# Kernel tuning notes

Measured on AMD Instinct MI355X. Metric: run time of the kernel, lower is better.

Reference implementation:

```python
import jax, jax.numpy as jnp
import numpy as np

NEG_SLOPE = 0.01

def lrelu(x):
    return jax.nn.leaky_relu(x, NEG_SLOPE)

def lin(x, w, b):
    # torch Linear: x @ W.T + b, W shape (out, in)
    return x @ w.T + b

def meansum_pool(mask, x_local, *x_global):
    # masked sum + mean over points, concat with global/context vectors
    x_sum = (x_local * mask).sum(axis=1)                 # (b, d)
    x_mean = x_sum / mask.sum(axis=1)                    # (b, d) / (b, 1)
    return jnp.concatenate([x_mean, x_sum, *x_global], axis=1)


def setup_inputs() -> dict:
    key = jax.random.key(0)
    ks = jax.random.split(key, 16)
    B, N, DIN, DC, H, G, NB, DOUT = 16, 8192, 3, 16, 128, 10, 6, 3

    def w(k, shape, fan_in):
        return (jax.random.normal(k, shape, jnp.float32) / np.float32(np.sqrt(fan_in)))

    inp = {
        "x_local": jax.random.normal(ks[0], (B, N, DIN), jnp.float32),
        "context": jax.random.normal(ks[1], (B, DC), jnp.float32),
        "mask": (jax.random.uniform(ks[2], (B, N, 1)) < 0.9).astype(jnp.float32),
        # EPiC_Projection params (effective weight-normed weights)
        "proj_lw": w(ks[3], (H, DIN), DIN), "proj_lb": jnp.zeros((H,), jnp.float32),
        "proj_g0w": w(ks[4], (H, 2 * H + DC), 2 * H + DC), "proj_g0b": jnp.zeros((H,), jnp.float32),
        "proj_g1w": w(ks[5], (H, H), H), "proj_g1b": jnp.zeros((H,), jnp.float32),
        "proj_g2w": w(ks[6], (G, H), H), "proj_g2b": jnp.zeros((G,), jnp.float32),
        # stacked per-block EPiC_layer params
        "g1w": w(ks[7], (NB, H, 2 * H + G + DC), 2 * H + G + DC), "g1b": jnp.zeros((NB, H), jnp.float32),
        "g2w": w(ks[8], (NB, G, H), H), "g2b": jnp.zeros((NB, G), jnp.float32),
        "l1w": w(ks[9], (NB, H, H + G + DC), H + G + DC), "l1b": jnp.zeros((NB, H), jnp.float32),
        "l2w": w(ks[10], (NB, H, H), H), "l2b": jnp.zeros((NB, H), jnp.float32),
        # output head
        "outw": w(ks[11], (DOUT, H), H), "outb": jnp.zeros((DOUT,), jnp.float32),
    }
    return inp


def reference(x_local, context, mask,
              proj_lw, proj_lb, proj_g0w, proj_g0b, proj_g1w, proj_g1b, proj_g2w, proj_g2b,
              g1w, g1b, g2w, g2b, l1w, l1b, l2w, l2b, outw, outb):
    B, N, _ = x_local.shape
    # --- EPiC_Projection ---
    xl = lrelu(lin(x_local, proj_lw, proj_lb))           # (b, n, H)
    xg = meansum_pool(mask, xl, context)                 # (b, 2H + DC)
    xg = lrelu(lin(xg, proj_g0w, proj_g0b))
    xg = lrelu(lin(xg, proj_g1w, proj_g1b))
    xg = lrelu(lin(xg, proj_g2w, proj_g2b))              # (b, G)
    xl = xl * mask
    # --- EPiC layers (no skip: use_skip_connection=False -> +0) ---
    num_blocks = g1w.shape[0]
    for i in range(num_blocks):
        pooled = meansum_pool(mask, xl, xg, context)     # (b, 2H + G + DC)
        h_g = lrelu(lin(pooled, g1w[i], g1b[i]))
        xg = lrelu(lin(h_g, g2w[i], g2b[i]) + xg)        # residual global
        xg_b = jnp.broadcast_to(xg[:, None, :], (B, N, xg.shape[-1]))
        ctx_b = jnp.broadcast_to(context[:, None, :], (B, N, context.shape[-1]))
        cat = jnp.concatenate([xl, xg_b, ctx_b], axis=2)  # (b, n, H + G + DC)
        h_l = lrelu(lin(cat, l1w[i], l1b[i]))
        xl = lrelu(lin(h_l, l2w[i], l2b[i]) + xl) * mask  # residual local, masked
    h = lin(xl, outw, outb)                              # (b, n, 3)
    return h * mask
```

## Files before the change

### kernel.cpp

```cpp
#include <hip/hip_runtime.h>
#include <hip/hip_bf16.h>


typedef __attribute__((ext_vector_type(8))) short short8;
typedef __attribute__((ext_vector_type(4))) float f32x4;

#define B_ 16
#define N_ 8192
#define DC_ 16
#define H_ 128
#define G_ 10
#define NB_ 6
#define NEG_ 0.01f

__device__ __forceinline__ float lrelu(float x) { return x > 0.f ? x : NEG_ * x; }

__device__ __forceinline__ unsigned short f2bf(float x) {
  union { float f; unsigned u; } v; v.f = x;
  return (unsigned short)((v.u + 0x7fffu + ((v.u >> 16) & 1u)) >> 16);
}
__device__ __forceinline__ float bf2f(unsigned short u) {
  union { unsigned u; float f; } v; v.u = ((unsigned)u) << 16; return v.f;
}
__device__ __forceinline__ void split_bf(float x, unsigned short& h, unsigned short& l) {
  union { float f; unsigned u; } v; v.f = x;
  unsigned hu = v.u & 0xffff0000u;
  h = (unsigned short)(hu >> 16);
  union { unsigned u; float f; } hv; hv.u = hu;
  l = f2bf(x - hv.f);
}

__device__ __forceinline__ f32x4 mfma16(short8 a, short8 b, f32x4 c) {
  return __builtin_amdgcn_mfma_f32_16x16x32_bf16(a, b, c, 0, 0, 0);
}

__device__ __forceinline__ void make_frags(f32x4 v0, f32x4 v1, short8& bh, short8& bl) {
  unsigned short h, l;
#pragma unroll
  for (int j = 0; j < 4; ++j) {
    split_bf(v0[j], h, l);
    bh[j] = (short)h; bl[j] = (short)l;
  }
#pragma unroll
  for (int j = 0; j < 4; ++j) {
    split_bf(v1[j], h, l);
    bh[4 + j] = (short)h; bl[4 + j] = (short)l;
  }
}

__device__ __forceinline__ void async_cp16(const void* g, void* l) {
  __builtin_amdgcn_global_load_lds(
      (const __attribute__((address_space(1))) void*)g,
      (__attribute__((address_space(3))) void*)l, 16, 0, 0);
}

__device__ __forceinline__ void agent_store(float* p, float v) {
  __hip_atomic_store(p, v, __ATOMIC_RELAXED, __HIP_MEMORY_SCOPE_AGENT);
}
__device__ __forceinline__ float agent_load(const float* p) {
  return __hip_atomic_load(p, __ATOMIC_RELAXED, __HIP_MEMORY_SCOPE_AGENT);
}

template <int NS>
__device__ void epic_global_tail(
    int b, int tid, const float* __restrict__ pP, float cnt,
    const float* __restrict__ xg_cur, float* __restrict__ xg_next,
    const float* __restrict__ context,
    const float* __restrict__ g1w_n, const float* __restrict__ g1b_n,
    const float* __restrict__ g2w_n, const float* __restrict__ g2b_n,
    const float* __restrict__ l1w_n, const float* __restrict__ l1b_n,
    float* __restrict__ gbias_out, float* shx) {
  if (tid < 256) {
    const int f = tid & 127, kh = tid >> 7;
    const float* pr = pP + ((size_t)b * NS + kh * (NS / 2)) * 128 + f;
    float s = 0.f;
#pragma unroll 8
    for (int w = 0; w < NS / 2; ++w) s += agent_load(pr + w * 128);
    shx[tid] = s;
  }
  __syncthreads();
  if (tid < 128) {
    float s = shx[tid] + shx[tid + 128];
    shx[384 + tid] = s;
    shx[256 + tid] = s / cnt;
  }
  if (tid < G_) shx[512 + tid] = xg_cur[tid];
  if (tid >= 32 && tid < 32 + DC_) shx[522 + tid - 32] = context[b * DC_ + tid - 32];
  __syncthreads();
  if (tid < 256) {
    const int f = tid & 127, kh = tid >> 7;
    const float* wr = g1w_n + (size_t)f * 282 + kh * 142;
    const float* vp = shx + 256 + kh * 142;
    const int n2 = kh ? 70 : 71;
    float a = 0.f;
#pragma unroll 8
    for (int j = 0; j < n2; ++j) {
      float2 w2 = *(const float2*)(wr + 2 * j);
      a += w2.x * vp[2 * j] + w2.y * vp[2 * j + 1];
    }
    shx[tid] = a;
  }
  __syncthreads();
  if (tid < 128) shx[544 + tid] = lrelu(shx[tid] + shx[tid + 128] + g1b_n[tid]);
  __syncthreads();
  if (tid < G_) {
    const float* wr = g2w_n + tid * 128;
    float a = g2b_n[tid] + shx[512 + tid];
#pragma unroll 8
    for (int j = 0; j < 32; ++j) {
      float4 w4 = *(const float4*)(wr + 4 * j);
      a += w4.x * shx[544 + 4 * j] + w4.y * shx[544 + 4 * j + 1] +
           w4.z * shx[544 + 4 * j + 2] + w4.w * shx[544 + 4 * j + 3];
    }
    float v = lrelu(a);
    shx[672 + tid] = v;
    xg_next[tid] = v;
  }
  __syncthreads();
  if (tid < 128) {
    const float* wr = l1w_n + tid * 154;
    float a = l1b_n[tid];
#pragma unroll
    for (int j = 0; j < G_; ++j) a += wr[128 + j] * shx[672 + j];
#pragma unroll
    for (int j = 0; j < DC_; ++j) a += wr[138 + j] * shx[522 + j];
    gbias_out[tid] = a;
  }
}

__global__ __launch_bounds__(256) void prep_weights(
    const float* __restrict__ l1w, const float* __restrict__ l2w,
    unsigned short* __restrict__ w1h, unsigned short* __restrict__ w1l,
    unsigned short* __restrict__ w2h, unsigned short* __restrict__ w2l,
    unsigned int* __restrict__ counters) {
  int idx = blockIdx.x * 256 + threadIdx.x;
  const int total = NB_ * H_ * H_;
  if (idx < 112) counters[idx] = 0u;
  if (idx < total) {
    int i = idx / (H_ * H_), rem = idx % (H_ * H_);
    int F = rem / H_, k = rem % H_;
    int mt = F >> 4, r = F & 15, ks = k >> 5, c = k & 31;
    int off = i * 16384 + (mt * 4 + ks) * 512 + ((c >> 3) * 16 + r) * 8 + (c & 7);
    unsigned short h, l;
    split_bf(l1w[(i * H_ + F) * 154 + k], h, l);
    w1h[off] = h; w1l[off] = l;
    split_bf(l2w[(i * H_ + F) * H_ + k], h, l);
    w2h[off] = h; w2l[off] = l;
  }
}

__global__ __launch_bounds__(256, 2) void proj_local_kernel(
    const float* __restrict__ xloc, const float* __restrict__ maskp,
    const float* __restrict__ plw, const float* __restrict__ plb,
    float* __restrict__ xlf, float* __restrict__ pP,
    float* __restrict__ cntp, float* __restrict__ cnt_g,
    unsigned int* __restrict__ counters,
    const float* __restrict__ context,
    const float* __restrict__ g0w, const float* __restrict__ g0b,
    const float* __restrict__ g1pw, const float* __restrict__ g1pb,
    const float* __restrict__ g2pw, const float* __restrict__ g2pb,
    float* __restrict__ xg_g,
    const float* __restrict__ g1w0, const float* __restrict__ g1b0,
    const float* __restrict__ g2w0, const float* __restrict__ g2b0,
    const float* __restrict__ l1w0, const float* __restrict__ l1b0,
    float* __restrict__ gbias_g) {
  __shared__ float wq[H_][4];
  __shared__ float wsum[512];
  __shared__ float cw[4];
  __shared__ float shx[768];
  __shared__ int winflag;
  const int tid = threadIdx.x, bid = blockIdx.x;
  const int wv = tid >> 6, lane = tid & 63;
  const int q = lane >> 4, n16 = lane & 15;
  const int b = bid >> 6;
  if (tid < H_) {
    wq[tid][0] = plw[tid * 3 + 0];
    wq[tid][1] = plw[tid * 3 + 1];
    wq[tid][2] = plw[tid * 3 + 2];
    wq[tid][3] = plb[tid];
  }
  __syncthreads();
  const int t = bid * 4 + wv;
  const int p0 = t * 32;
  const int pa = p0 + n16, pb = p0 + 16 + n16;
  const float xa0 = xloc[pa * 3], xa1 = xloc[pa * 3 + 1], xa2 = xloc[pa * 3 + 2];
  const float xb0 = xloc[pb * 3], xb1 = xloc[pb * 3 + 1], xb2 = xloc[pb * 3 + 2];
  const float m0 = maskp[pa], m1 = maskp[pb];
  float* ga = xlf + (size_t)(2 * t) * 2048;
  float* gb = ga + 2048;
#pragma unroll
  for (int ms = 0; ms < 8; ++ms) {
    f32x4 v0, v1;
#pragma unroll
    for (int r = 0; r < 4; ++r) {
      const int F = ms * 16 + q * 4 + r;
      float4 w4 = *(const float4*)wq[F];
      v0[r] = lrelu(w4.x * xa0 + w4.y * xa1 + w4.z * xa2 + w4.w) * m0;
      v1[r] = lrelu(w4.x * xb0 + w4.y * xb1 + w4.z * xb2 + w4.w) * m1;
    }
    *(f32x4*)(ga + ms * 256 + (q * 16 + n16) * 4) = v0;
    *(f32x4*)(gb + ms * 256 + (q * 16 + n16) * 4) = v1;
    f32x4 s = v0 + v1;
#pragma unroll
    for (int r = 0; r < 4; ++r) {
      float sv = s[r];
      sv += __shfl_xor(sv, 1, 64);
      sv += __shfl_xor(sv, 2, 64);
      sv += __shfl_xor(sv, 4, 64);
      sv += __shfl_xor(sv, 8, 64);
      s[r] = sv;
    }
    if (n16 == 0) *(f32x4*)&wsum[wv * 128 + ms * 16 + q * 4] = s;
  }
  {
    float c = (q == 0) ? (m0 + m1) : 0.f;
    c += __shfl_xor(c, 1, 64);
    c += __shfl_xor(c, 2, 64);
    c += __shfl_xor(c, 4, 64);
    c += __shfl_xor(c, 8, 64);
    if (lane == 0) cw[wv] = c;
  }
  __syncthreads();
  if (tid < 128) {
    agent_store(&pP[(size_t)(2 * bid) * 128 + tid], wsum[tid] + wsum[128 + tid]);
    agent_store(&pP[(size_t)(2 * bid + 1) * 128 + tid], wsum[256 + tid] + wsum[384 + tid]);
  }
  if (tid == 0) agent_store(&cntp[bid], cw[0] + cw[1] + cw[2] + cw[3]);

  __syncthreads();
  if (tid == 0) winflag = (atomicAdd(&counters[b], 1u) == 63u) ? 1 : 0;
  __syncthreads();
  if (!winflag) return;
  if (tid < 64) shx[688 + tid] = agent_load(&cntp[b * 64 + tid]);
  __syncthreads();
  if (tid == 0) {
    float c = 0.f;
#pragma unroll
    for (int w = 0; w < 64; ++w) c += shx[688 + w];
    shx[752] = c;
    cnt_g[b] = c;
  }
  __syncthreads();
  const float cnt = shx[752];
  {
    const int f = tid & 127, kh = tid >> 7;
    const float* pr = pP + ((size_t)b * 128 + kh * 64) * 128 + f;
    float s = 0.f;
#pragma unroll 8
    for (int w = 0; w < 64; ++w) s += agent_load(pr + w * 128);
    shx[tid] = s;
  }
  __syncthreads();
  if (tid < 128) {
    float s = shx[tid] + shx[tid + 128];
    shx[384 + tid] = s;
    shx[256 + tid] = s / cnt;
  }
  if (tid < DC_) shx[512 + tid] = context[b * DC_ + tid];
  __syncthreads();
  {
    const int f = tid & 127, kh = tid >> 7;
    const float* wr = g0w + (size_t)f * 272 + kh * 136;
    const float* vp = shx + 256 + kh * 136;
    float a = 0.f;
#pragma unroll 8
    for (int j = 0; j < 34; ++j) {
      float4 w4 = *(const float4*)(wr + 4 * j);
      a += w4.x * vp[4 * j] + w4.y * vp[4 * j + 1] + w4.z * vp[4 * j + 2] + w4.w * vp[4 * j + 3];
    }
    __syncthreads();
    shx[tid] = a;
  }
  __syncthreads();
  if (tid < 128) shx[544 + tid] = lrelu(shx[tid] + shx[tid + 128] + g0b[tid]);
  __syncthreads();
  {
    const int f = tid & 127, kh = tid >> 7;
    const float* wr = g1pw + (size_t)f * 128 + kh * 64;
    const float* vp = shx + 544 + kh * 64;
    float a = 0.f;
#pragma unroll 8
    for (int j = 0; j < 16; ++j) {
      float4 w4 = *(const float4*)(wr + 4 * j);
      a += w4.x * vp[4 * j] + w4.y * vp[4 * j + 1] + w4.z * vp[4 * j + 2] + w4.w * vp[4 * j + 3];
    }
    __syncthreads();
    shx[tid] = a;
  }
  __syncthreads();
  if (tid < 128) shx[544 + tid] = lrelu(shx[tid] + shx[tid + 128] + g1pb[tid]);
  __syncthreads();
  if (tid < G_) {
    const float* wr = g2pw + tid * 128;
    float a = g2pb[tid];
#pragma unroll 8
    for (int j = 0; j < 32; ++j) {
      float4 w4 = *(const float4*)(wr + 4 * j);
      a += w4.x * shx[544 + 4 * j] + w4.y * shx[544 + 4 * j + 1] +
           w4.z * shx[544 + 4 * j + 2] + w4.w * shx[544 + 4 * j + 3];
    }
    xg_g[(0 * 16 + b) * 16 + tid] = lrelu(a);
  }
  __syncthreads();
  epic_global_tail<128>(b, tid, pP, cnt,
                        xg_g + (0 * 16 + b) * 16, xg_g + (1 * 16 + b) * 16, context,
                        g1w0, g1b0, g2w0, g2b0, l1w0, l1b0,
                        gbias_g + (size_t)(0 * 16 + b) * 128, shx);
}

template <bool LAST>
__global__ __launch_bounds__(512, 2) void epic_local_kernel(
    float* __restrict__ xlf, float* __restrict__ pP,
    const float* __restrict__ cnt_g, unsigned int* __restrict__ counters_blk,
    const float* __restrict__ gbias_in,
    const float* __restrict__ xg_tail_cur, float* __restrict__ xg_tail_next,
    float* __restrict__ gbias_tail_out,
    const float* __restrict__ context,
    const float* __restrict__ g1w_n, const float* __restrict__ g1b_n,
    const float* __restrict__ g2w_n, const float* __restrict__ g2b_n,
    const float* __restrict__ l1w_n, const float* __restrict__ l1b_n,
    const float* __restrict__ l2b,
    const unsigned short* __restrict__ w1h, const unsigned short* __restrict__ w1l,
    const unsigned short* __restrict__ w2h, const unsigned short* __restrict__ w2l,
    const float* __restrict__ maskp,
    const float* __restrict__ outw, const float* __restrict__ outb,
    float* __restrict__ outp) {
  __shared__ unsigned short wbuf[65536];
  __shared__ float tiles[8][576];
  __shared__ float shx[768];
  __shared__ float gbias_s[128];
  __shared__ float l2b_s[128];
  __shared__ float wsum[1024];
  __shared__ float outw_s[392];
  __shared__ int winflag;
  const int tid = threadIdx.x, bid = blockIdx.x;
  const int b = bid >> 5;
  const int wv = tid >> 6, lane = tid & 63;
  const int q = lane >> 4, n16 = lane & 15;

  {
    const unsigned short* src =
        (wv < 2) ? w1h : (wv < 4) ? w1l : (wv < 6) ? w2h : w2l;
    const char* s8 = (const char*)(src + (wv & 1) * 8192) + lane * 16;
    char* d8 = (char*)wbuf + wv * 16384;
#pragma unroll
    for (int j = 0; j < 16; ++j) async_cp16(s8 + j * 1024, d8 + j * 1024);
  }
  if (tid < 128) {
    gbias_s[tid] = gbias_in[b * 128 + tid];
    l2b_s[tid] = l2b[tid];
  }
  if (LAST) {
    if (tid < 384) outw_s[tid] = outw[tid];
    if (tid >= 384 && tid < 387) outw_s[tid] = outb[tid - 384];
  }

  const int g0i = bid * 16 + wv * 2;
  short8 xbh[2][4], xbl[2][4];
#pragma unroll
  for (int nt = 0; nt < 2; ++nt) {
    const float* base_nt = xlf + (size_t)(g0i + nt) * 2048;
#pragma unroll
    for (int ks = 0; ks < 4; ++ks) {
      const float* pb = base_nt + (2 * ks + (q >> 1)) * 256 + ((q & 1) * 32 + n16) * 4;
      f32x4 v0 = *(const f32x4*)pb;
      f32x4 v1 = *(const f32x4*)(pb + 64);
      make_frags(v0, v1, xbh[nt][ks], xbl[nt][ks]);
    }
  }
  __syncthreads();

  const unsigned short* w1h_l = wbuf;
  const unsigned short* w1l_l = wbuf + 16384;
  const unsigned short* w2h_l = wbuf + 32768;
  const unsigned short* w2l_l = wbuf + 49152;
  float* T = tiles[wv];
  const int lane16 = lane * 8;

  f32x4 acc2[2][8];
#pragma unroll
  for (int nt = 0; nt < 2; ++nt)
#pragma unroll
    for (int ms = 0; ms < 8; ++ms) acc2[nt][ms] = (f32x4){0.f, 0.f, 0.f, 0.f};

#pragma unroll
  for (int ko = 0; ko < 4; ++ko) {
    f32x4 acc[2][2];
#pragma unroll
    for (int nt = 0; nt < 2; ++nt)
#pragma unroll
      for (int msl = 0; msl < 2; ++msl) acc[nt][msl] = (f32x4){0.f, 0.f, 0.f, 0.f};
#pragma unroll
    for (int msl = 0; msl < 2; ++msl) {
      short8 a1h[4], a1l[4];
#pragma unroll
      for (int ks = 0; ks < 4; ++ks) {
        const int off = ((ko * 2 + msl) * 4 + ks) * 512 + lane16;
        a1h[ks] = *(const short8*)(w1h_l + off);
        a1l[ks] = *(const short8*)(w1l_l + off);
      }
#pragma unroll
      for (int ks = 0; ks < 4; ++ks)
#pragma unroll
        for (int nt = 0; nt < 2; ++nt) {
          acc[nt][msl] = mfma16(a1h[ks], xbh[nt][ks], acc[nt][msl]);
          acc[nt][msl] = mfma16(a1l[ks], xbh[nt][ks], acc[nt][msl]);
          acc[nt][msl] = mfma16(a1h[ks], xbl[nt][ks], acc[nt][msl]);
        }
    }
    short8 b2h[2], b2l[2];
#pragma unroll
    for (int nt = 0; nt < 2; ++nt) {
#pragma unroll
      for (int msl = 0; msl < 2; ++msl) {
        f32x4 gb4 = *(const f32x4*)&gbias_s[(ko * 2 + msl) * 16 + q * 4];
        f32x4 hv;
#pragma unroll
        for (int r = 0; r < 4; ++r) hv[r] = lrelu(acc[nt][msl][r] + gb4[r]);
        *(f32x4*)&T[n16 * 36 + msl * 16 + q * 4] = hv;
      }
      __builtin_amdgcn_wave_barrier();
      {
        f32x4 h0 = *(const f32x4*)&T[n16 * 36 + q * 8];
        f32x4 h1 = *(const f32x4*)&T[n16 * 36 + q * 8 + 4];
        make_frags(h0, h1, b2h[nt], b2l[nt]);
      }
      __builtin_amdgcn_wave_barrier();
    }
#pragma unroll
    for (int half = 0; half < 2; ++half) {
      short8 a2h[4], a2l[4];
#pragma unroll
      for (int mi = 0; mi < 4; ++mi) {
        const int off = ((half * 4 + mi) * 4 + ko) * 512 + lane16;
        a2h[mi] = *(const short8*)(w2h_l + off);
        a2l[mi] = *(const short8*)(w2l_l + off);
      }
#pragma unroll
      for (int mi = 0; mi < 4; ++mi)
#pragma unroll
        for (int nt = 0; nt < 2; ++nt) {
          acc2[nt][half * 4 + mi] = mfma16(a2h[mi], b2h[nt], acc2[nt][half * 4 + mi]);
          acc2[nt][half * 4 + mi] = mfma16(a2l[mi], b2h[nt], acc2[nt][half * 4 + mi]);
          acc2[nt][half * 4 + mi] = mfma16(a2h[mi], b2l[nt], acc2[nt][half * 4 + mi]);
        }
    }
  }

  float mk[2];
#pragma unroll
  for (int nt = 0; nt < 2; ++nt) mk[nt] = maskp[(g0i + nt) * 16 + n16];
  f32x4 vsum[8];
  float po[2][3];
  if (!LAST) {
#pragma unroll
    for (int ms = 0; ms < 8; ++ms) vsum[ms] = (f32x4){0.f, 0.f, 0.f, 0.f};
  } else {
#pragma unroll
    for (int nt = 0; nt < 2; ++nt) po[nt][0] = po[nt][1] = po[nt][2] = 0.f;
  }
#pragma unroll
  for (int nt = 0; nt < 2; ++nt) {
    float* base_nt = xlf + (size_t)(g0i + nt) * 2048;
#pragma unroll
    for (int ms = 0; ms < 8; ++ms) {
      f32x4 lb4 = *(const f32x4*)&l2b_s[ms * 16 + q * 4];
      float* xo = base_nt + ms * 256 + (q * 16 + n16) * 4;
      f32x4 old = *(const f32x4*)xo;
      f32x4 v;
#pragma unroll
      for (int r = 0; r < 4; ++r) v[r] = lrelu(acc2[nt][ms][r] + lb4[r] + old[r]) * mk[nt];
      if (!LAST) {
        *(f32x4*)xo = v;
        vsum[ms] += v;
      } else {
        f32x4 w0 = *(const f32x4*)&outw_s[0 * 128 + ms * 16 + q * 4];
        f32x4 w1 = *(const f32x4*)&outw_s[1 * 128 + ms * 16 + q * 4];
        f32x4 w2 = *(const f32x4*)&outw_s[2 * 128 + ms * 16 + q * 4];
#pragma unroll
        for (int r = 0; r < 4; ++r) {
          po[nt][0] += v[r] * w0[r];
          po[nt][1] += v[r] * w1[r];
          po[nt][2] += v[r] * w2[r];
        }
      }
    }
  }
  if (LAST) {
#pragma unroll
    for (int nt = 0; nt < 2; ++nt)
#pragma unroll
      for (int o = 0; o < 3; ++o) {
        float s = po[nt][o];
        s += __shfl_xor(s, 16, 64);
        s += __shfl_xor(s, 32, 64);
        po[nt][o] = s;
      }
    if (q == 0) {
#pragma unroll
      for (int nt = 0; nt < 2; ++nt) {
        const int p = (g0i + nt) * 16 + n16;
#pragma unroll
        for (int o = 0; o < 3; ++o)
          outp[(size_t)p * 3 + o] = (po[nt][o] + outw_s[384 + o]) * mk[nt];
      }
    }
    return;
  }
#pragma unroll
  for (int ms = 0; ms < 8; ++ms) {
    f32x4 sr;
#pragma unroll
    for (int r = 0; r < 4; ++r) {
      float s = vsum[ms][r];
      s += __shfl_xor(s, 1, 64);
      s += __shfl_xor(s, 2, 64);
      s += __shfl_xor(s, 4, 64);
      s += __shfl_xor(s, 8, 64);
      sr[r] = s;
    }
    if (n16 == 0) *(f32x4*)&wsum[wv * 128 + ms * 16 + q * 4] = sr;
  }
  __syncthreads();
  if (tid < 128) {
    float s = 0.f;
#pragma unroll
    for (int w = 0; w < 8; ++w) s += wsum[w * 128 + tid];
    agent_store(&pP[(size_t)bid * 128 + tid], s);
  }

  __syncthreads();
  if (tid == 0) winflag = (atomicAdd(&counters_blk[b], 1u) == 31u) ? 1 : 0;
  __syncthreads();
  if (!winflag) return;
  epic_global_tail<32>(b, tid, pP, cnt_g[b], xg_tail_cur + b * 16, xg_tail_next + b * 16,
                       context, g1w_n, g1b_n, g2w_n, g2b_n, l1w_n, l1b_n,
                       gbias_tail_out + (size_t)b * 128, shx);
}

extern "C" void kernel_launch(void* const* d_in, const int* in_sizes, int n_in,
                              void* d_out, int out_size, void* d_ws, size_t ws_size,
                              hipStream_t stream) {
  const float* x_local = (const float*)d_in[0];
  const float* context = (const float*)d_in[1];
  const float* mask = (const float*)d_in[2];
  const float* proj_lw = (const float*)d_in[3];
  const float* proj_lb = (const float*)d_in[4];
  const float* proj_g0w = (const float*)d_in[5];
  const float* proj_g0b = (const float*)d_in[6];
  const float* proj_g1w = (const float*)d_in[7];
  const float* proj_g1b = (const float*)d_in[8];
  const float* proj_g2w = (const float*)d_in[9];
  const float* proj_g2b = (const float*)d_in[10];
  const float* g1w = (const float*)d_in[11];
  const float* g1b = (const float*)d_in[12];
  const float* g2w = (const float*)d_in[13];
  const float* g2b = (const float*)d_in[14];
  const float* l1w = (const float*)d_in[15];
  const float* l1b = (const float*)d_in[16];
  const float* l2w = (const float*)d_in[17];
  const float* l2b = (const float*)d_in[18];
  const float* outw = (const float*)d_in[19];
  const float* outb = (const float*)d_in[20];
  float* out = (float*)d_out;

  char* ws = (char*)d_ws;
  float* xlf = (float*)ws;
  float* pP = (float*)(ws + 67108864);
  float* cntp = (float*)(ws + 68157440);
  float* cnt_g = (float*)(ws + 68161536);
  float* xg_g = (float*)(ws + 68161600);
  float* gbias_g = (float*)(ws + 68168768);
  unsigned int* counters = (unsigned int*)(ws + 68217920);
  unsigned short* w1h = (unsigned short*)(ws + 68218368);
  unsigned short* w1l = (unsigned short*)(ws + 68414976);
  unsigned short* w2h = (unsigned short*)(ws + 68611584);
  unsigned short* w2l = (unsigned short*)(ws + 68808192);

  prep_weights<<<384, 256, 0, stream>>>(l1w, l2w, w1h, w1l, w2h, w2l, counters);
  proj_local_kernel<<<1024, 256, 0, stream>>>(
      x_local, mask, proj_lw, proj_lb, xlf, pP, cntp, cnt_g, counters, context,
      proj_g0w, proj_g0b, proj_g1w, proj_g1b, proj_g2w, proj_g2b, xg_g,
      g1w, g1b, g2w, g2b, l1w, l1b, gbias_g);
  for (int i = 0; i < NB_; ++i) {
    const int j = i + 1;
    const float* g1w_n = g1w + (size_t)j * 128 * 282;
    const float* g1b_n = g1b + j * 128;
    const float* g2w_n = g2w + j * 10 * 128;
    const float* g2b_n = g2b + j * 10;
    const float* l1w_n = l1w + (size_t)j * 128 * 154;
    const float* l1b_n = l1b + j * 128;
    const unsigned short* w1h_i = w1h + i * 16384;
    const unsigned short* w1l_i = w1l + i * 16384;
    const unsigned short* w2h_i = w2h + i * 16384;
    const unsigned short* w2l_i = w2l + i * 16384;
    if (i == NB_ - 1) {
      epic_local_kernel<true><<<512, 512, 0, stream>>>(
          xlf, pP, cnt_g, counters + (i + 1) * 16, gbias_g + (size_t)(i * 16) * 128,
          nullptr, nullptr, nullptr, context,
          nullptr, nullptr, nullptr, nullptr, nullptr, nullptr,
          l2b + i * 128, w1h_i, w1l_i, w2h_i, w2l_i, mask, outw, outb, out);
    } else {
      epic_local_kernel<false><<<512, 512, 0, stream>>>(
          xlf, pP, cnt_g, counters + (i + 1) * 16, gbias_g + (size_t)(i * 16) * 128,
          xg_g + (i + 1) * 16 * 16, xg_g + (i + 2) * 16 * 16,
          gbias_g + (size_t)((i + 1) * 16) * 128, context,
          g1w_n, g1b_n, g2w_n, g2b_n, l1w_n, l1b_n,
          l2b + i * 128, w1h_i, w1l_i, w2h_i, w2l_i, mask, outw, outb, out);
    }
  }
}
```

Baseline: 477.1 us.

## Process two point tiles per block and pass hidden layer via cross-lane shuffles

Halves the grid so each block loops over two 256-point tiles, amortizing the 128KB LDS weight load and reducing global partial sums and atomic counters per batch. The first GEMM now computes all 8 output tiles before the second GEMM, and the intermediate activations are redistributed between MFMA layouts with __shfl instead of a per-wave LDS tile, removing the tiles buffer and its wave barriers. This raises register pressure (full acc[2][8] plus b2 fragments) and adds many shuffle instructions, and the smaller grid means fewer blocks to hide latency.

```diff
diff --git a/kernel.cpp b/kernel.cpp
--- a/kernel.cpp
+++ b/kernel.cpp
@@ -326,7 +326,6 @@
     const float* __restrict__ outw, const float* __restrict__ outb,
     float* __restrict__ outp) {
   __shared__ unsigned short wbuf[65536];
-  __shared__ float tiles[8][576];
   __shared__ float shx[768];
   __shared__ float gbias_s[128];
   __shared__ float l2b_s[128];
@@ -334,7 +333,7 @@
   __shared__ float outw_s[392];
   __shared__ int winflag;
   const int tid = threadIdx.x, bid = blockIdx.x;
-  const int b = bid >> 5;
+  const int b = bid >> 4;
   const int wv = tid >> 6, lane = tid & 63;
   const int q = lane >> 4, n16 = lane & 15;
 
@@ -354,159 +353,173 @@
     if (tid < 384) outw_s[tid] = outw[tid];
     if (tid >= 384 && tid < 387) outw_s[tid] = outb[tid - 384];
   }
-
-  const int g0i = bid * 16 + wv * 2;
-  short8 xbh[2][4], xbl[2][4];
-#pragma unroll
-  for (int nt = 0; nt < 2; ++nt) {
-    const float* base_nt = xlf + (size_t)(g0i + nt) * 2048;
-#pragma unroll
-    for (int ks = 0; ks < 4; ++ks) {
-      const float* pb = base_nt + (2 * ks + (q >> 1)) * 256 + ((q & 1) * 32 + n16) * 4;
-      f32x4 v0 = *(const f32x4*)pb;
-      f32x4 v1 = *(const f32x4*)(pb + 64);
-      make_frags(v0, v1, xbh[nt][ks], xbl[nt][ks]);
-    }
-  }
   __syncthreads();
 
   const unsigned short* w1h_l = wbuf;
   const unsigned short* w1l_l = wbuf + 16384;
   const unsigned short* w2h_l = wbuf + 32768;
   const unsigned short* w2l_l = wbuf + 49152;
-  float* T = tiles[wv];
   const int lane16 = lane * 8;
-
-  f32x4 acc2[2][8];
-#pragma unroll
-  for (int nt = 0; nt < 2; ++nt)
-#pragma unroll
-    for (int ms = 0; ms < 8; ++ms) acc2[nt][ms] = (f32x4){0.f, 0.f, 0.f, 0.f};
-
-#pragma unroll
-  for (int ko = 0; ko < 4; ++ko) {
-    f32x4 acc[2][2];
+  const int srcA = 2 * (q & 1) * 16 + n16;
+  const bool sel = (q >> 1) != 0;
+
+  f32x4 vsum[8];
+  if (!LAST) {
+#pragma unroll
+    for (int ms = 0; ms < 8; ++ms) vsum[ms] = (f32x4){0.f, 0.f, 0.f, 0.f};
+  }
+
+#pragma unroll
+  for (int it = 0; it < 2; ++it) {
+    const int g0i = (bid * 2 + it) * 16 + wv * 2;
+
+    short8 xbh[2][4], xbl[2][4];
+#pragma unroll
+    for (int nt = 0; nt < 2; ++nt) {
+      const float* base_nt = xlf + (size_t)(g0i + nt) * 2048;
+#pragma unroll
+      for (int ks = 0; ks < 4; ++ks) {
+        const float* pb = base_nt + (2 * ks + (q >> 1)) * 256 + ((q & 1) * 32 + n16) * 4;
+        f32x4 v0 = *(const f32x4*)pb;
+        f32x4 v1 = *(const f32x4*)(pb + 64);
+        make_frags(v0, v1, xbh[nt][ks], xbl[nt][ks]);
+      }
+    }
+
+    f32x4 acc[2][8];
 #pragma unroll
     for (int nt = 0; nt < 2; ++nt)
 #pragma unroll
-      for (int msl = 0; msl < 2; ++msl) acc[nt][msl] = (f32x4){0.f, 0.f, 0.f, 0.f};
-#pragma unroll
-    for (int msl = 0; msl < 2; ++msl) {
-      short8 a1h[4], a1l[4];
+      for (int mt = 0; mt < 8; ++mt) acc[nt][mt] = (f32x4){0.f, 0.f, 0.f, 0.f};
+#pragma unroll
+    for (int mt = 0; mt < 8; ++mt) {
+      short8 ah[4], al[4];
 #pragma unroll
       for (int ks = 0; ks < 4; ++ks) {
-        const int off = ((ko * 2 + msl) * 4 + ks) * 512 + lane16;
-        a1h[ks] = *(const short8*)(w1h_l + off);
-        a1l[ks] = *(const short8*)(w1l_l + off);
+        const int off = (mt * 4 + ks) * 512 + lane16;
+        ah[ks] = *(const short8*)(w1h_l + off);
+        al[ks] = *(const short8*)(w1l_l + off);
       }
 #pragma unroll
       for (int ks = 0; ks < 4; ++ks)
 #pragma unroll
         for (int nt = 0; nt < 2; ++nt) {
-          acc[nt][msl] = mfma16(a1h[ks], xbh[nt][ks], acc[nt][msl]);
-          acc[nt][msl] = mfma16(a1l[ks], xbh[nt][ks], acc[nt][msl]);
-          acc[nt][msl] = mfma16(a1h[ks], xbl[nt][ks], acc[nt][msl]);
+          acc[nt][mt] = mfma16(ah[ks], xbh[nt][ks], acc[nt][mt]);
+          acc[nt][mt] = mfma16(al[ks], xbh[nt][ks], acc[nt][mt]);
+          acc[nt][mt] = mfma16(ah[ks], xbl[nt][ks], acc[nt][mt]);
         }
     }
-    short8 b2h[2], b2l[2];
+
+#pragma unroll
+    for (int mt = 0; mt < 8; ++mt) {
+      f32x4 gb4 = *(const f32x4*)&gbias_s[mt * 16 + q * 4];
+#pragma unroll
+      for (int nt = 0; nt < 2; ++nt)
+#pragma unroll
+        for (int r = 0; r < 4; ++r) acc[nt][mt][r] = lrelu(acc[nt][mt][r] + gb4[r]);
+    }
+
+    short8 b2h[2][4], b2l[2][4];
+#pragma unroll
+    for (int nt = 0; nt < 2; ++nt)
+#pragma unroll
+      for (int ks = 0; ks < 4; ++ks) {
+        f32x4 f0, f1;
+#pragma unroll
+        for (int r = 0; r < 4; ++r) {
+          float a0 = __shfl(acc[nt][2 * ks][r], srcA, 64);
+          float a1 = __shfl(acc[nt][2 * ks + 1][r], srcA, 64);
+          f0[r] = sel ? a1 : a0;
+          float c0 = __shfl(acc[nt][2 * ks][r], srcA + 16, 64);
+          float c1 = __shfl(acc[nt][2 * ks + 1][r], srcA + 16, 64);
+          f1[r] = sel ? c1 : c0;
+        }
+        make_frags(f0, f1, b2h[nt][ks], b2l[nt][ks]);
+      }
+
+    f32x4 acc2[2][8];
+#pragma unroll
+    for (int nt = 0; nt < 2; ++nt)
+#pragma unroll
+      for (int mt = 0; mt < 8; ++mt) acc2[nt][mt] = (f32x4){0.f, 0.f, 0.f, 0.f};
+#pragma unroll
+    for (int mt = 0; mt < 8; ++mt) {
+      short8 ah[4], al[4];
+#pragma unroll
+      for (int ks = 0; ks < 4; ++ks) {
+        const int off = (mt * 4 + ks) * 512 + lane16;
+        ah[ks] = *(const short8*)(w2h_l + off);
+        al[ks] = *(const short8*)(w2l_l + off);
+      }
+#pragma unroll
+      for (int ks = 0; ks < 4; ++ks)
+#pragma unroll
+        for (int nt = 0; nt < 2; ++nt) {
+          acc2[nt][mt] = mfma16(ah[ks], b2h[nt][ks], acc2[nt][mt]);
+          acc2[nt][mt] = mfma16(al[ks], b2h[nt][ks], acc2[nt][mt]);
+          acc2[nt][mt] = mfma16(ah[ks], b2l[nt][ks], acc2[nt][mt]);
+        }
+    }
+
+    float mk[2];
+#pragma unroll
+    for (int nt = 0; nt < 2; ++nt) mk[nt] = maskp[(g0i + nt) * 16 + n16];
+    float po[2][3];
+    if (LAST) {
+#pragma unroll
+      for (int nt = 0; nt < 2; ++nt) po[nt][0] = po[nt][1] = po[nt][2] = 0.f;
+    }
 #pragma unroll
     for (int nt = 0; nt < 2; ++nt) {
-#pragma unroll
-      for (int msl = 0; msl < 2; ++msl) {
-        f32x4 gb4 = *(const f32x4*)&gbias_s[(ko * 2 + msl) * 16 + q * 4];
-        f32x4 hv;
-#pragma unroll
-        for (int r = 0; r < 4; ++r) hv[r] = lrelu(acc[nt][msl][r] + gb4[r]);
-        *(f32x4*)&T[n16 * 36 + msl * 16 + q * 4] = hv;
-      }
-      __builtin_amdgcn_wave_barrier();
-      {
-        f32x4 h0 = *(const f32x4*)&T[n16 * 36 + q * 8];
-        f32x4 h1 = *(const f32x4*)&T[n16 * 36 + q * 8 + 4];
-        make_frags(h0, h1, b2h[nt], b2l[nt]);
-      }
-      __builtin_amdgcn_wave_barrier();
-    }
-#pragma unroll
-    for (int half = 0; half < 2; ++half) {
-      short8 a2h[4], a2l[4];
-#pragma unroll
-      for (int mi = 0; mi < 4; ++mi) {
-        const int off = ((half * 4 + mi) * 4 + ko) * 512 + lane16;
-        a2h[mi] = *(const short8*)(w2h_l + off);
-        a2l[mi] = *(const short8*)(w2l_l + off);
-      }
-#pragma unroll
-      for (int mi = 0; mi < 4; ++mi)
-#pragma unroll
-        for (int nt = 0; nt < 2; ++nt) {
-          acc2[nt][half * 4 + mi] = mfma16(a2h[mi], b2h[nt], acc2[nt][half * 4 + mi]);
-          acc2[nt][half * 4 + mi] = mfma16(a2l[mi], b2h[nt], acc2[nt][half * 4 + mi]);
-          acc2[nt][half * 4 + mi] = mfma16(a2h[mi], b2l[nt], acc2[nt][half * 4 + mi]);
-        }
-    }
-  }
-
-  float mk[2];
-#pragma unroll
-  for (int nt = 0; nt < 2; ++nt) mk[nt] = maskp[(g0i + nt) * 16 + n16];
-  f32x4 vsum[8];
-  float po[2][3];
-  if (!LAST) {
-#pragma unroll
-    for (int ms = 0; ms < 8; ++ms) vsum[ms] = (f32x4){0.f, 0.f, 0.f, 0.f};
-  } else {
-#pragma unroll
-    for (int nt = 0; nt < 2; ++nt) po[nt][0] = po[nt][1] = po[nt][2] = 0.f;
-  }
-#pragma unroll
-  for (int nt = 0; nt < 2; ++nt) {
-    float* base_nt = xlf + (size_t)(g0i + nt) * 2048;
-#pragma unroll
-    for (int ms = 0; ms < 8; ++ms) {
-      f32x4 lb4 = *(const f32x4*)&l2b_s[ms * 16 + q * 4];
-      float* xo = base_nt + ms * 256 + (q * 16 + n16) * 4;
-      f32x4 old = *(const f32x4*)xo;
-      f32x4 v;
-#pragma unroll
-      for (int r = 0; r < 4; ++r) v[r] = lrelu(acc2[nt][ms][r] + lb4[r] + old[r]) * mk[nt];
-      if (!LAST) {
-        *(f32x4*)xo = v;
-        vsum[ms] += v;
-      } else {
-        f32x4 w0 = *(const f32x4*)&outw_s[0 * 128 + ms * 16 + q * 4];
-        f32x4 w1 = *(const f32x4*)&outw_s[1 * 128 + ms * 16 + q * 4];
-        f32x4 w2 = *(const f32x4*)&outw_s[2 * 128 + ms * 16 + q * 4];
-#pragma unroll
-        for (int r = 0; r < 4; ++r) {
-          po[nt][0] += v[r] * w0[r];
-          po[nt][1] += v[r] * w1[r];
-          po[nt][2] += v[r] * w2[r];
+      float* base_nt = xlf + (size_t)(g0i + nt) * 2048;
+#pragma unroll
+      for (int ms = 0; ms < 8; ++ms) {
+        f32x4 lb4 = *(const f32x4*)&l2b_s[ms * 16 + q * 4];
+        float* xo = base_nt + ms * 256 + (q * 16 + n16) * 4;
+        f32x4 old = *(const f32x4*)xo;
+        f32x4 v;
+#pragma unroll
+        for (int r = 0; r < 4; ++r) v[r] = lrelu(acc2[nt][ms][r] + lb4[r] + old[r]) * mk[nt];
+        if (!LAST) {
+          *(f32x4*)xo = v;
+          vsum[ms] += v;
+        } else {
+          f32x4 w0 = *(const f32x4*)&outw_s[0 * 128 + ms * 16 + q * 4];
+          f32x4 w1 = *(const f32x4*)&outw_s[1 * 128 + ms * 16 + q * 4];
+          f32x4 w2 = *(const f32x4*)&outw_s[2 * 128 + ms * 16 + q * 4];
+#pragma unroll
+          for (int r = 0; r < 4; ++r) {
+            po[nt][0] += v[r] * w0[r];
+            po[nt][1] += v[r] * w1[r];
+            po[nt][2] += v[r] * w2[r];
+          }
         }
       }
     }
-  }
-  if (LAST) {
-#pragma unroll
-    for (int nt = 0; nt < 2; ++nt)
-#pragma unroll
-      for (int o = 0; o < 3; ++o) {
-        float s = po[nt][o];
-        s += __shfl_xor(s, 16, 64);
-        s += __shfl_xor(s, 32, 64);
-        po[nt][o] = s;
+    if (LAST) {
+#pragma unroll
+      for (int nt = 0; nt < 2; ++nt)
+#pragma unroll
+        for (int o = 0; o < 3; ++o) {
+          float s = po[nt][o];
+          s += __shfl_xor(s, 16, 64);
+          s += __shfl_xor(s, 32, 64);
+          po[nt][o] = s;
+        }
+      if (q == 0) {
+#pragma unroll
+        for (int nt = 0; nt < 2; ++nt) {
+          const int p = (g0i + nt) * 16 + n16;
+#pragma unroll
+          for (int o = 0; o < 3; ++o)
+            outp[(size_t)p * 3 + o] = (po[nt][o] + outw_s[384 + o]) * mk[nt];
+        }
       }
-    if (q == 0) {
-#pragma unroll
-      for (int nt = 0; nt < 2; ++nt) {
-        const int p = (g0i + nt) * 16 + n16;
-#pragma unroll
-        for (int o = 0; o < 3; ++o)
-          outp[(size_t)p * 3 + o] = (po[nt][o] + outw_s[384 + o]) * mk[nt];
-      }
-    }
-    return;
-  }
+    }
+  }
+
+  if (LAST) return;
+
 #pragma unroll
   for (int ms = 0; ms < 8; ++ms) {
     f32x4 sr;
@@ -530,10 +543,10 @@
   }
 
   __syncthreads();
-  if (tid == 0) winflag = (atomicAdd(&counters_blk[b], 1u) == 31u) ? 1 : 0;
+  if (tid == 0) winflag = (atomicAdd(&counters_blk[b], 1u) == 15u) ? 1 : 0;
   __syncthreads();
   if (!winflag) return;
-  epic_global_tail<32>(b, tid, pP, cnt_g[b], xg_tail_cur + b * 16, xg_tail_next + b * 16,
+  epic_global_tail<16>(b, tid, pP, cnt_g[b], xg_tail_cur + b * 16, xg_tail_next + b * 16,
                        context, g1w_n, g1b_n, g2w_n, g2b_n, l1w_n, l1b_n,
                        gbias_tail_out + (size_t)b * 128, shx);
 }
@@ -595,13 +608,13 @@
     const unsigned short* w2h_i = w2h + i * 16384;
     const unsigned short* w2l_i = w2l + i * 16384;
     if (i == NB_ - 1) {
-      epic_local_kernel<true><<<512, 512, 0, stream>>>(
+      epic_local_kernel<true><<<256, 512, 0, stream>>>(
           xlf, pP, cnt_g, counters + (i + 1) * 16, gbias_g + (size_t)(i * 16) * 128,
           nullptr, nullptr, nullptr, context,
           nullptr, nullptr, nullptr, nullptr, nullptr, nullptr,
           l2b + i * 128, w1h_i, w1l_i, w2h_i, w2l_i, mask, outw, outb, out);
     } else {
-      epic_local_kernel<false><<<512, 512, 0, stream>>>(
+      epic_local_kernel<false><<<256, 512, 0, stream>>>(
           xlf, pP, cnt_g, counters + (i + 1) * 16, gbias_g + (size_t)(i * 16) * 128,
           xg_g + (i + 1) * 16 * 16, xg_g + (i + 2) * 16 * 16,
           gbias_g + (size_t)((i + 1) * 16) * 128, context,
```

Measured after the change: 578.3 us. 21.2% more time.

## Store activations as pre-split bf16 hi/lo fragments and process two tiles per block

Applied to the files above, without the earlier changes.

The per-point activation buffer changes from fp32 to two bf16 arrays (hi and lo parts), laid out so each lane can load MFMA B-fragments directly. This removes the fp32-to-fragment conversion in every layer. Each epic_local block now handles two point-group iterations, so half as many blocks are launched and each block loads its LDS weights once for twice the work. The tail counter and reduction width are adjusted to match. The hi+lo split keeps roughly fp32 precision, but the residual is now rounded through the split representation on every layer.

```diff
diff --git a/kernel.cpp b/kernel.cpp
--- a/kernel.cpp
+++ b/kernel.cpp
@@ -3,6 +3,7 @@
 
 
 typedef __attribute__((ext_vector_type(8))) short short8;
+typedef __attribute__((ext_vector_type(4))) short short4v;
 typedef __attribute__((ext_vector_type(4))) float f32x4;
 
 #define B_ 16
@@ -152,7 +153,8 @@
 __global__ __launch_bounds__(256, 2) void proj_local_kernel(
     const float* __restrict__ xloc, const float* __restrict__ maskp,
     const float* __restrict__ plw, const float* __restrict__ plb,
-    float* __restrict__ xlf, float* __restrict__ pP,
+    unsigned short* __restrict__ xlh, unsigned short* __restrict__ xll,
+    float* __restrict__ pP,
     float* __restrict__ cntp, float* __restrict__ cnt_g,
     unsigned int* __restrict__ counters,
     const float* __restrict__ context,
@@ -186,8 +188,8 @@
   const float xa0 = xloc[pa * 3], xa1 = xloc[pa * 3 + 1], xa2 = xloc[pa * 3 + 2];
   const float xb0 = xloc[pb * 3], xb1 = xloc[pb * 3 + 1], xb2 = xloc[pb * 3 + 2];
   const float m0 = maskp[pa], m1 = maskp[pb];
-  float* ga = xlf + (size_t)(2 * t) * 2048;
-  float* gb = ga + 2048;
+  const size_t ga = (size_t)(2 * t) * 2048;
+  const size_t gb = ga + 2048;
 #pragma unroll
   for (int ms = 0; ms < 8; ++ms) {
     f32x4 v0, v1;
@@ -198,8 +200,18 @@
       v0[r] = lrelu(w4.x * xa0 + w4.y * xa1 + w4.z * xa2 + w4.w) * m0;
       v1[r] = lrelu(w4.x * xb0 + w4.y * xb1 + w4.z * xb2 + w4.w) * m1;
     }
-    *(f32x4*)(ga + ms * 256 + (q * 16 + n16) * 4) = v0;
-    *(f32x4*)(gb + ms * 256 + (q * 16 + n16) * 4) = v1;
+    const int off = (ms * 2 + (q >> 1)) * 128 + n16 * 8 + (q & 1) * 4;
+    short4v h0, l0, h1, l1;
+#pragma unroll
+    for (int r = 0; r < 4; ++r) {
+      unsigned short h, l;
+      split_bf(v0[r], h, l); h0[r] = (short)h; l0[r] = (short)l;
+      split_bf(v1[r], h, l); h1[r] = (short)h; l1[r] = (short)l;
+    }
+    *(short4v*)(xlh + ga + off) = h0;
+    *(short4v*)(xll + ga + off) = l0;
+    *(short4v*)(xlh + gb + off) = h1;
+    *(short4v*)(xll + gb + off) = l1;
     f32x4 s = v0 + v1;
 #pragma unroll
     for (int r = 0; r < 4; ++r) {
@@ -310,7 +322,8 @@
 
 template <bool LAST>
 __global__ __launch_bounds__(512, 2) void epic_local_kernel(
-    float* __restrict__ xlf, float* __restrict__ pP,
+    unsigned short* __restrict__ xlh, unsigned short* __restrict__ xll,
+    float* __restrict__ pP,
     const float* __restrict__ cnt_g, unsigned int* __restrict__ counters_blk,
     const float* __restrict__ gbias_in,
     const float* __restrict__ xg_tail_cur, float* __restrict__ xg_tail_next,
@@ -334,7 +347,7 @@
   __shared__ float outw_s[392];
   __shared__ int winflag;
   const int tid = threadIdx.x, bid = blockIdx.x;
-  const int b = bid >> 5;
+  const int b = bid >> 4;
   const int wv = tid >> 6, lane = tid & 63;
   const int q = lane >> 4, n16 = lane & 15;
 
@@ -353,20 +366,6 @@
   if (LAST) {
     if (tid < 384) outw_s[tid] = outw[tid];
     if (tid >= 384 && tid < 387) outw_s[tid] = outb[tid - 384];
-  }
-
-  const int g0i = bid * 16 + wv * 2;
-  short8 xbh[2][4], xbl[2][4];
-#pragma unroll
-  for (int nt = 0; nt < 2; ++nt) {
-    const float* base_nt = xlf + (size_t)(g0i + nt) * 2048;
-#pragma unroll
-    for (int ks = 0; ks < 4; ++ks) {
-      const float* pb = base_nt + (2 * ks + (q >> 1)) * 256 + ((q & 1) * 32 + n16) * 4;
-      f32x4 v0 = *(const f32x4*)pb;
-      f32x4 v1 = *(const f32x4*)(pb + 64);
-      make_frags(v0, v1, xbh[nt][ks], xbl[nt][ks]);
-    }
   }
   __syncthreads();
 
@@ -377,136 +376,169 @@
   float* T = tiles[wv];
   const int lane16 = lane * 8;
 
-  f32x4 acc2[2][8];
-#pragma unroll
-  for (int nt = 0; nt < 2; ++nt)
-#pragma unroll
-    for (int ms = 0; ms < 8; ++ms) acc2[nt][ms] = (f32x4){0.f, 0.f, 0.f, 0.f};
-
-#pragma unroll
-  for (int ko = 0; ko < 4; ++ko) {
-    f32x4 acc[2][2];
+  f32x4 vsum[8];
+  if (!LAST) {
+#pragma unroll
+    for (int ms = 0; ms < 8; ++ms) vsum[ms] = (f32x4){0.f, 0.f, 0.f, 0.f};
+  }
+
+#pragma unroll
+  for (int it = 0; it < 2; ++it) {
+    const int g0i = (bid * 2 + it) * 16 + wv * 2;
+
+    short8 xbh[2][4], xbl[2][4];
+#pragma unroll
+    for (int nt = 0; nt < 2; ++nt) {
+      const size_t gbase = (size_t)(g0i + nt) * 2048;
+#pragma unroll
+      for (int ks = 0; ks < 4; ++ks) {
+        const size_t off = gbase + (ks * 4 + q) * 128 + n16 * 8;
+        xbh[nt][ks] = *(const short8*)(xlh + off);
+        xbl[nt][ks] = *(const short8*)(xll + off);
+      }
+    }
+
+    f32x4 acc2[2][8];
 #pragma unroll
     for (int nt = 0; nt < 2; ++nt)
 #pragma unroll
-      for (int msl = 0; msl < 2; ++msl) acc[nt][msl] = (f32x4){0.f, 0.f, 0.f, 0.f};
-#pragma unroll
-    for (int msl = 0; msl < 2; ++msl) {
-      short8 a1h[4], a1l[4];
-#pragma unroll
-      for (int ks = 0; ks < 4; ++ks) {
-        const int off = ((ko * 2 + msl) * 4 + ks) * 512 + lane16;
-        a1h[ks] = *(const short8*)(w1h_l + off);
-        a1l[ks] = *(const short8*)(w1l_l + off);
+      for (int ms = 0; ms < 8; ++ms) acc2[nt][ms] = (f32x4){0.f, 0.f, 0.f, 0.f};
+
+#pragma unroll
+    for (int ko = 0; ko < 4; ++ko) {
+      f32x4 acc[2][2];
+#pragma unroll
+      for (int nt = 0; nt < 2; ++nt)
+#pragma unroll
+        for (int msl = 0; msl < 2; ++msl) acc[nt][msl] = (f32x4){0.f, 0.f, 0.f, 0.f};
+#pragma unroll
+      for (int msl = 0; msl < 2; ++msl) {
+        short8 a1h[4], a1l[4];
+#pragma unroll
+        for (int ks = 0; ks < 4; ++ks) {
+          const int off = ((ko * 2 + msl) * 4 + ks) * 512 + lane16;
+          a1h[ks] = *(const short8*)(w1h_l + off);
+          a1l[ks] = *(const short8*)(w1l_l + off);
+        }
+#pragma unroll
+        for (int ks = 0; ks < 4; ++ks)
+#pragma unroll
+          for (int nt = 0; nt < 2; ++nt) {
+            acc[nt][msl] = mfma16(a1h[ks], xbh[nt][ks], acc[nt][msl]);
+            acc[nt][msl] = mfma16(a1l[ks], xbh[nt][ks], acc[nt][msl]);
+            acc[nt][msl] = mfma16(a1h[ks], xbl[nt][ks], acc[nt][msl]);
+          }
       }
-#pragma unroll
-      for (int ks = 0; ks < 4; ++ks)
+      short8 b2h[2], b2l[2];
+#pragma unroll
+      for (int nt = 0; nt < 2; ++nt) {
+#pragma unroll
+        for (int msl = 0; msl < 2; ++msl) {
+          f32x4 gb4 = *(const f32x4*)&gbias_s[(ko * 2 + msl) * 16 + q * 4];
+          f32x4 hv;
+#pragma unroll
+          for (int r = 0; r < 4; ++r) hv[r] = lrelu(acc[nt][msl][r] + gb4[r]);
+          *(f32x4*)&T[n16 * 36 + msl * 16 + q * 4] = hv;
+        }
+        __builtin_amdgcn_wave_barrier();
+        {
+          f32x4 h0 = *(const f32x4*)&T[n16 * 36 + q * 8];
+          f32x4 h1 = *(const f32x4*)&T[n16 * 36 + q * 8 + 4];
+          make_frags(h0, h1, b2h[nt], b2l[nt]);
+        }
+        __builtin_amdgcn_wave_barrier();
+      }
+#pragma unroll
+      for (int half = 0; half < 2; ++half) {
+        short8 a2h[4], a2l[4];
+#pragma unroll
+        for (int mi = 0; mi < 4; ++mi) {
+          const int off = ((half * 4 + mi) * 4 + ko) * 512 + lane16;
+          a2h[mi] = *(const short8*)(w2h_l + off);
+          a2l[mi] = *(const short8*)(w2l_l + off);
+        }
+#pragma unroll
+        for (int mi = 0; mi < 4; ++mi)
+#pragma unroll
+          for (int nt = 0; nt < 2; ++nt) {
+            acc2[nt][half * 4 + mi] = mfma16(a2h[mi], b2h[nt], acc2[nt][half * 4 + mi]);
+            acc2[nt][half * 4 + mi] = mfma16(a2l[mi], b2h[nt], acc2[nt][half * 4 + mi]);
+            acc2[nt][half * 4 + mi] = mfma16(a2h[mi], b2l[nt], acc2[nt][half * 4 + mi]);
+          }
+      }
+    }
+
+    float mk[2];
+#pragma unroll
+    for (int nt = 0; nt < 2; ++nt) mk[nt] = maskp[(g0i + nt) * 16 + n16];
+    float po[2][3];
+    if (LAST) {
+#pragma unroll
+      for (int nt = 0; nt < 2; ++nt) po[nt][0] = po[nt][1] = po[nt][2] = 0.f;
+    }
+#pragma unroll
+    for (int nt = 0; nt < 2; ++nt) {
+      const size_t gbase = (size_t)(g0i + nt) * 2048;
+#pragma unroll
+      for (int ms = 0; ms < 8; ++ms) {
+        f32x4 lb4 = *(const f32x4*)&l2b_s[ms * 16 + q * 4];
+        const int off = (ms * 2 + (q >> 1)) * 128 + n16 * 8 + (q & 1) * 4;
+        short4v oh = *(const short4v*)(xlh + gbase + off);
+        short4v ol = *(const short4v*)(xll + gbase + off);
+        f32x4 v;
+#pragma unroll
+        for (int r = 0; r < 4; ++r) {
+          float old = bf2f((unsigned short)oh[r]) + bf2f((unsigned short)ol[r]);
+          v[r] = lrelu(acc2[nt][ms][r] + lb4[r] + old) * mk[nt];
+        }
+        if (!LAST) {
+          short4v nh, nl;
+#pragma unroll
+          for (int r = 0; r < 4; ++r) {
+            unsigned short h, l;
+            split_bf(v[r], h, l);
+            nh[r] = (short)h; nl[r] = (short)l;
+          }
+          *(short4v*)(xlh + gbase + off) = nh;
+          *(short4v*)(xll + gbase + off) = nl;
+          vsum[ms] += v;
+        } else {
+          f32x4 w0 = *(const f32x4*)&outw_s[0 * 128 + ms * 16 + q * 4];
+          f32x4 w1 = *(const f32x4*)&outw_s[1 * 128 + ms * 16 + q * 4];
+          f32x4 w2 = *(const f32x4*)&outw_s[2 * 128 + ms * 16 + q * 4];
+#pragma unroll
+          for (int r = 0; r < 4; ++r) {
+            po[nt][0] += v[r] * w0[r];
+            po[nt][1] += v[r] * w1[r];
+            po[nt][2] += v[r] * w2[r];
+          }
+        }
+      }
+    }
+    if (LAST) {
+#pragma unroll
+      for (int nt = 0; nt < 2; ++nt)
+#pragma unroll
+        for (int o = 0; o < 3; ++o) {
+          float s = po[nt][o];
+          s += __shfl_xor(s, 16, 64);
+          s += __shfl_xor(s, 32, 64);
+          po[nt][o] = s;
+        }
+      if (q == 0) {
 #pragma unroll
         for (int nt = 0; nt < 2; ++nt) {
-          acc[nt][msl] = mfma16(a1h[ks], xbh[nt][ks], acc[nt][msl]);
-          acc[nt][msl] = mfma16(a1l[ks], xbh[nt][ks], acc[nt][msl]);
-          acc[nt][msl] = mfma16(a1h[ks], xbl[nt][ks], acc[nt][msl]);
-        }
-    }
-    short8 b2h[2], b2l[2];
-#pragma unroll
-    for (int nt = 0; nt < 2; ++nt) {
-#pragma unroll
-      for (int msl = 0; msl < 2; ++msl) {
-        f32x4 gb4 = *(const f32x4*)&gbias_s[(ko * 2 + msl) * 16 + q * 4];
-        f32x4 hv;
-#pragma unroll
-        for (int r = 0; r < 4; ++r) hv[r] = lrelu(acc[nt][msl][r] + gb4[r]);
-        *(f32x4*)&T[n16 * 36 + msl * 16 + q * 4] = hv;
+          const int p = (g0i + nt) * 16 + n16;
+#pragma unroll
+          for (int o = 0; o < 3; ++o)
+            outp[(size_t)p * 3 + o] = (po[nt][o] + outw_s[384 + o]) * mk[nt];
+        }
       }
-      __builtin_amdgcn_wave_barrier();
-      {
-        f32x4 h0 = *(const f32x4*)&T[n16 * 36 + q * 8];
-        f32x4 h1 = *(const f32x4*)&T[n16 * 36 + q * 8 + 4];
-        make_frags(h0, h1, b2h[nt], b2l[nt]);
-      }
-      __builtin_amdgcn_wave_barrier();
-    }
-#pragma unroll
-    for (int half = 0; half < 2; ++half) {
-      short8 a2h[4], a2l[4];
-#pragma unroll
-      for (int mi = 0; mi < 4; ++mi) {
-        const int off = ((half * 4 + mi) * 4 + ko) * 512 + lane16;
-        a2h[mi] = *(const short8*)(w2h_l + off);
-        a2l[mi] = *(const short8*)(w2l_l + off);
-      }
-#pragma unroll
-      for (int mi = 0; mi < 4; ++mi)
-#pragma unroll
-        for (int nt = 0; nt < 2; ++nt) {
-          acc2[nt][half * 4 + mi] = mfma16(a2h[mi], b2h[nt], acc2[nt][half * 4 + mi]);
-          acc2[nt][half * 4 + mi] = mfma16(a2l[mi], b2h[nt], acc2[nt][half * 4 + mi]);
-          acc2[nt][half * 4 + mi] = mfma16(a2h[mi], b2l[nt], acc2[nt][half * 4 + mi]);
-        }
-    }
-  }
-
-  float mk[2];
-#pragma unroll
-  for (int nt = 0; nt < 2; ++nt) mk[nt] = maskp[(g0i + nt) * 16 + n16];
-  f32x4 vsum[8];
-  float po[2][3];
-  if (!LAST) {
-#pragma unroll
-    for (int ms = 0; ms < 8; ++ms) vsum[ms] = (f32x4){0.f, 0.f, 0.f, 0.f};
-  } else {
-#pragma unroll
-    for (int nt = 0; nt < 2; ++nt) po[nt][0] = po[nt][1] = po[nt][2] = 0.f;
-  }
-#pragma unroll
-  for (int nt = 0; nt < 2; ++nt) {
-    float* base_nt = xlf + (size_t)(g0i + nt) * 2048;
-#pragma unroll
-    for (int ms = 0; ms < 8; ++ms) {
-      f32x4 lb4 = *(const f32x4*)&l2b_s[ms * 16 + q * 4];
-      float* xo = base_nt + ms * 256 + (q * 16 + n16) * 4;
-      f32x4 old = *(const f32x4*)xo;
-      f32x4 v;
-#pragma unroll
-      for (int r = 0; r < 4; ++r) v[r] = lrelu(acc2[nt][ms][r] + lb4[r] + old[r]) * mk[nt];
-      if (!LAST) {
-        *(f32x4*)xo = v;
-        vsum[ms] += v;
-      } else {
-        f32x4 w0 = *(const f32x4*)&outw_s[0 * 128 + ms * 16 + q * 4];
-        f32x4 w1 = *(const f32x4*)&outw_s[1 * 128 + ms * 16 + q * 4];
-        f32x4 w2 = *(const f32x4*)&outw_s[2 * 128 + ms * 16 + q * 4];
-#pragma unroll
-        for (int r = 0; r < 4; ++r) {
-          po[nt][0] += v[r] * w0[r];
-          po[nt][1] += v[r] * w1[r];
-          po[nt][2] += v[r] * w2[r];
-        }
-      }
-    }
-  }
-  if (LAST) {
-#pragma unroll
-    for (int nt = 0; nt < 2; ++nt)
-#pragma unroll
-      for (int o = 0; o < 3; ++o) {
-        float s = po[nt][o];
-        s += __shfl_xor(s, 16, 64);
-        s += __shfl_xor(s, 32, 64);
-        po[nt][o] = s;
-      }
-    if (q == 0) {
-#pragma unroll
-      for (int nt = 0; nt < 2; ++nt) {
-        const int p = (g0i + nt) * 16 + n16;
-#pragma unroll
-        for (int o = 0; o < 3; ++o)
-          outp[(size_t)p * 3 + o] = (po[nt][o] + outw_s[384 + o]) * mk[nt];
-      }
-    }
-    return;
-  }
+    }
+  }
+
+  if (LAST) return;
+
 #pragma unroll
   for (int ms = 0; ms < 8; ++ms) {
     f32x4 sr;
@@ -530,10 +562,10 @@
   }
 
   __syncthreads();
-  if (tid == 0) winflag = (atomicAdd(&counters_blk[b], 1u) == 31u) ? 1 : 0;
+  if (tid == 0) winflag = (atomicAdd(&counters_blk[b], 1u) == 15u) ? 1 : 0;
   __syncthreads();
   if (!winflag) return;
-  epic_global_tail<32>(b, tid, pP, cnt_g[b], xg_tail_cur + b * 16, xg_tail_next + b * 16,
+  epic_global_tail<16>(b, tid, pP, cnt_g[b], xg_tail_cur + b * 16, xg_tail_next + b * 16,
                        context, g1w_n, g1b_n, g2w_n, g2b_n, l1w_n, l1b_n,
                        gbias_tail_out + (size_t)b * 128, shx);
 }
@@ -565,7 +597,8 @@
   float* out = (float*)d_out;
 
   char* ws = (char*)d_ws;
-  float* xlf = (float*)ws;
+  unsigned short* xlh = (unsigned short*)ws;
+  unsigned short* xll = (unsigned short*)(ws + 33554432);
   float* pP = (float*)(ws + 67108864);
   float* cntp = (float*)(ws + 68157440);
   float* cnt_g = (float*)(ws + 68161536);
@@ -579,7 +612,7 @@
 
   prep_weights<<<384, 256, 0, stream>>>(l1w, l2w, w1h, w1l, w2h, w2l, counters);
   proj_local_kernel<<<1024, 256, 0, stream>>>(
-      x_local, mask, proj_lw, proj_lb, xlf, pP, cntp, cnt_g, counters, context,
+      x_local, mask, proj_lw, proj_lb, xlh, xll, pP, cntp, cnt_g, counters, context,
       proj_g0w, proj_g0b, proj_g1w, proj_g1b, proj_g2w, proj_g2b, xg_g,
       g1w, g1b, g2w, g2b, l1w, l1b, gbias_g);
   for (int i = 0; i < NB_; ++i) {
@@ -595,14 +628,14 @@
     const unsigned short* w2h_i = w2h + i * 16384;
     const unsigned short* w2l_i = w2l + i * 16384;
     if (i == NB_ - 1) {
-      epic_local_kernel<true><<<512, 512, 0, stream>>>(
-          xlf, pP, cnt_g, counters + (i + 1) * 16, gbias_g + (size_t)(i * 16) * 128,
+      epic_local_kernel<true><<<256, 512, 0, stream>>>(
+          xlh, xll, pP, cnt_g, counters + (i + 1) * 16, gbias_g + (size_t)(i * 16) * 128,
           nullptr, nullptr, nullptr, context,
           nullptr, nullptr, nullptr, nullptr, nullptr, nullptr,
           l2b + i * 128, w1h_i, w1l_i, w2h_i, w2l_i, mask, outw, outb, out);
     } else {
-      epic_local_kernel<false><<<512, 512, 0, stream>>>(
-          xlf, pP, cnt_g, counters + (i + 1) * 16, gbias_g + (size_t)(i * 16) * 128,
+      epic_local_kernel<false><<<256, 512, 0, stream>>>(
+          xlh, xll, pP, cnt_g, counters + (i + 1) * 16, gbias_g + (size_t)(i * 16) * 128,
           xg_g + (i + 1) * 16 * 16, xg_g + (i + 2) * 16 * 16,
           gbias_g + (size_t)((i + 1) * 16) * 128, context,
           g1w_n, g1b_n, g2w_n, g2b_n, l1w_n, l1b_n,
```

New measurement: 497.7 us. +4.3%, slower.
